# Performance work log

Measured on AMD Instinct MI355X. Metric: run time of the kernel, lower is better.

The kernel has to match this reference:

```python
import jax, jax.numpy as jnp
import numpy as np
import math

T, B, D, H, L, C = 2048, 64, 256, 256, 2, 2
HIGHWAY_BIAS = 0.0
# SRU rescale factor for the highway skip term (rescale=True)
SCALE_X = (1.0 + math.exp(HIGHWAY_BIAS * 2)) ** 0.5


def setup_inputs() -> dict:
    key = jax.random.key(0)
    ks = jax.random.split(key, 8)
    s = 1.0 / np.sqrt(D)
    x = jax.random.normal(ks[0], (T, B, D), dtype=jnp.float32)
    # per-layer SRU weights: W [D, 3H] -> (x_tilde, f, r); bias [2H] -> (b_f, b_r)
    W1 = jax.random.uniform(ks[1], (D, 3 * H), jnp.float32, -s, s)
    b1 = jnp.zeros((2 * H,), jnp.float32)
    W2 = jax.random.uniform(ks[2], (H, 3 * H), jnp.float32, -s, s)
    b2 = jnp.zeros((2 * H,), jnp.float32)
    lin_W = jax.random.uniform(ks[3], (H, C), jnp.float32, -s, s)
    lin_b = jnp.zeros((C,), jnp.float32)
    return {"x": x, "W1": W1, "b1": b1, "W2": W2, "b2": b2,
            "lin_W": lin_W, "lin_b": lin_b}


def _sru_layer(x, W, b):
    # x: [T, B, D]; W: [D, 3H]; b: [2H]. Skip term uses raw x (D == H).
    U = jnp.einsum('tbd,dk->tbk', x, W)           # [T, B, 3H]
    x_tilde, f_raw, r_raw = jnp.split(U, 3, axis=-1)
    b_f, b_r = jnp.split(b, 2)
    f = jax.nn.sigmoid(f_raw + b_f + HIGHWAY_BIAS)  # [T, B, H]
    r = jax.nn.sigmoid(r_raw + b_r)                 # [T, B, H]

    def step(c, inp):
        f_t, xt_t = inp
        c = f_t * c + (1.0 - f_t) * xt_t
        return c, c

    c0 = jnp.zeros(x.shape[1:], x.dtype)            # [B, H]
    _, cs = jax.lax.scan(step, c0, (f, x_tilde))    # cs: [T, B, H]
    h = r * cs + (1.0 - r) * (x * SCALE_X)          # highway skip (rescaled)
    return h


def reference(x, W1, b1, W2, b2, lin_W, lin_b):
    h1 = _sru_layer(x, W1, b1)
    h2 = _sru_layer(h1, W2, b2)
    last = h2[-1]                                   # [B, H] (last timestep)
    # Dropout in eval mode = identity (deterministic reference)
    return last @ lin_W + lin_b                     # [B, C]
```

## Files before the change

kernel.cpp:

```cpp
#include <hip/hip_runtime.h>
#include <hip/hip_bf16.h>
#include <stdint.h>

#define T_LEN 2048
#define B_SZ  64
#define H_SZ  256
#define NH3   768
#define M_SZ  (T_LEN * B_SZ)
#define NC    64
#define TC    32
#define SCALE_X_F 1.41421356237309515f

typedef __attribute__((ext_vector_type(8))) short short8;
typedef __attribute__((ext_vector_type(4))) float f32x4;

__device__ __forceinline__ float sigmoidf_(float z) {
    return 1.0f / (1.0f + __expf(-z));
}
__device__ __forceinline__ unsigned short f2bf(float f) {
    unsigned u = __float_as_uint(f);
    return (unsigned short)((u + 0x7FFFu + ((u >> 16) & 1u)) >> 16);
}
__device__ __forceinline__ float bf2f(unsigned short s) {
    return __uint_as_float(((unsigned)s) << 16);
}

__global__ void k_convert_x(const float* __restrict__ x, unsigned short* __restrict__ xb) {
    int i = blockIdx.x * blockDim.x + threadIdx.x;
    const float4* in = (const float4*)x;
    float4 a = in[i * 2];
    float4 b = in[i * 2 + 1];
    short8 o;
    o[0] = (short)f2bf(a.x); o[1] = (short)f2bf(a.y);
    o[2] = (short)f2bf(a.z); o[3] = (short)f2bf(a.w);
    o[4] = (short)f2bf(b.x); o[5] = (short)f2bf(b.y);
    o[6] = (short)f2bf(b.z); o[7] = (short)f2bf(b.w);
    *(short8*)&xb[(size_t)i * 8] = o;
}

__global__ void k_prep_w(const float* __restrict__ W, unsigned short* __restrict__ Wt) {
    int i = blockIdx.x * 256 + threadIdx.x;
    int n = i >> 8, k = i & 255;
    Wt[i] = f2bf(W[(size_t)k * NH3 + n]);
}

template <int NT, int CS, int TPB>
__global__ void __launch_bounds__(256, 2)
k_gemm(const unsigned short* __restrict__ A,
       const unsigned short* __restrict__ Bt,
       unsigned short* __restrict__ C) {
    __shared__ alignas(16) unsigned short lds[2][16384];

    int orig = blockIdx.x;
    int wgid = (orig & 7) * 64 + (orig >> 3);
    int t0 = wgid * TPB;

    int tid = threadIdx.x;
    int w = tid >> 6, l = tid & 63;
    int r16 = l & 15, kg = l >> 4;
    int wr = w >> 1, wc = w & 1;
    int scol = ((l & 7) ^ (l >> 3)) * 8;
    int srow = (l >> 3);

    auto stage = [&](int t, int kt, int b) {
        int mb = (t / NT) * 128, nb = (t % NT) * 128;
        #pragma unroll
        for (int p = 0; p < 4; ++p) {
            int row = w * 32 + p * 8 + srow;
            const unsigned short* ga = A  + (size_t)(mb + row) * 256 + kt * 64 + scol;
            const unsigned short* gb = Bt + (size_t)(nb + row) * 256 + kt * 64 + scol;
            __builtin_amdgcn_global_load_lds(
                (const __attribute__((address_space(1))) void*)ga,
                (__attribute__((address_space(3))) void*)&lds[b][(w * 4 + p) * 512], 16, 0, 0);
            __builtin_amdgcn_global_load_lds(
                (const __attribute__((address_space(1))) void*)gb,
                (__attribute__((address_space(3))) void*)&lds[b][8192 + (w * 4 + p) * 512], 16, 0, 0);
        }
    };

    stage(t0, 0, 0);

    #pragma unroll 1
    for (int i = 0; i < TPB; ++i) {
        int t = t0 + i;

        f32x4 acc[4][4];
        #pragma unroll
        for (int m = 0; m < 4; ++m)
            #pragma unroll
            for (int n = 0; n < 4; ++n) {
                f32x4 z = {0.f, 0.f, 0.f, 0.f};
                acc[m][n] = z;
            }

        #pragma unroll
        for (int kt = 0; kt < 4; ++kt) {
            if (kt < 3) stage(t, kt + 1, (kt + 1) & 1);
            else        stage(min(t + 1, t0 + TPB - 1), 0, 0);

            asm volatile("s_waitcnt vmcnt(8)" ::: "memory");
            __builtin_amdgcn_s_barrier();
            asm volatile("" ::: "memory");

            const unsigned short* As = &lds[kt & 1][0];
            const unsigned short* Bs = &lds[kt & 1][8192];
            short8 af[4][2], bfv[4][2];
            #pragma unroll
            for (int m = 0; m < 4; ++m) {
                int arow = wr * 64 + m * 16 + r16;
                int sw = (arow & 7) << 3;
                #pragma unroll
                for (int kk = 0; kk < 2; ++kk)
                    af[m][kk] = *(const short8*)&As[arow * 64 + ((kk * 32 + kg * 8) ^ sw)];
            }
            #pragma unroll
            for (int n = 0; n < 4; ++n) {
                int brow = wc * 64 + n * 16 + r16;
                int sw = (brow & 7) << 3;
                #pragma unroll
                for (int kk = 0; kk < 2; ++kk)
                    bfv[n][kk] = *(const short8*)&Bs[brow * 64 + ((kk * 32 + kg * 8) ^ sw)];
            }

            __builtin_amdgcn_s_setprio(1);
            #pragma unroll
            for (int m = 0; m < 4; ++m)
                #pragma unroll
                for (int n = 0; n < 4; ++n)
                    #pragma unroll
                    for (int kk = 0; kk < 2; ++kk)
                        acc[m][n] = __builtin_amdgcn_mfma_f32_16x16x32_bf16(
                            af[m][kk], bfv[n][kk], acc[m][n], 0, 0, 0);
            __builtin_amdgcn_s_setprio(0);

            asm volatile("" ::: "memory");
            __builtin_amdgcn_s_barrier();
            asm volatile("" ::: "memory");
        }

        unsigned short* ep = &lds[1][0];
        int mbase = (t / NT) * 128, nbase = (t % NT) * 128;
        #pragma unroll
        for (int m = 0; m < 4; ++m)
            #pragma unroll
            for (int n = 0; n < 4; ++n) {
                int col = wc * 64 + n * 16 + r16;
                #pragma unroll
                for (int r = 0; r < 4; ++r) {
                    int row = wr * 64 + m * 16 + kg * 4 + r;
                    ep[row * 128 + (col ^ ((row & 7) << 3))] = f2bf(acc[m][n][r]);
                }
            }
        asm volatile("s_waitcnt lgkmcnt(0)" ::: "memory");
        __builtin_amdgcn_s_barrier();
        asm volatile("" ::: "memory");
        #pragma unroll
        for (int s = 0; s < 8; ++s) {
            int slot = s * 256 + tid;
            int row = slot >> 4, seg = slot & 15;
            short8 v = *(const short8*)&ep[row * 128 + ((seg * 8) ^ ((row & 7) << 3))];
            *(short8*)&C[(size_t)(mbase + row) * CS + nbase + seg * 8] = v;
        }
        asm volatile("s_waitcnt lgkmcnt(0)" ::: "memory");
        __builtin_amdgcn_s_barrier();
        asm volatile("" ::: "memory");
    }
}

__global__ void k_passA(const unsigned short* __restrict__ U, const float* __restrict__ bias,
                        float* __restrict__ P, float* __restrict__ S, int stride) {
    int ci = blockIdx.x >> 6;
    int b  = blockIdx.x & 63;
    int h  = threadIdx.x;
    float bfv = bias[h];
    size_t base = ((size_t)(ci * TC) * B_SZ + b) * stride + h;
    float c = 0.f, pr = 1.f;
    #pragma unroll 4
    for (int t = 0; t < TC; ++t) {
        float xt = bf2f(U[base]);
        float fr = bf2f(U[base + 256]);
        float f = sigmoidf_(fr + bfv);
        c = f * c + (1.f - f) * xt;
        pr *= f;
        base += (size_t)B_SZ * stride;
    }
    int o = blockIdx.x * 256 + h;
    P[o] = pr;
    S[o] = c;
}

__global__ void k_passB(const float* __restrict__ P, const float* __restrict__ S,
                        float* __restrict__ cin) {
    int b = blockIdx.x, h = threadIdx.x;
    int idx = b * 256 + h;
    float c = 0.f;
    #pragma unroll 8
    for (int ci = 0; ci < NC; ++ci) {
        cin[ci * 16384 + idx] = c;
        c = P[ci * 16384 + idx] * c + S[ci * 16384 + idx];
    }
    cin[NC * 16384 + idx] = c;
}

__global__ void k_passC(const unsigned short* __restrict__ U, const float* __restrict__ bias,
                        const unsigned short* __restrict__ xb, const float* __restrict__ cin,
                        unsigned short* __restrict__ hout) {
    int ci = blockIdx.x >> 6, b = blockIdx.x & 63, h = threadIdx.x;
    float bfv = bias[h], brv = bias[256 + h];
    float c = cin[blockIdx.x * 256 + h];
    size_t base  = ((size_t)(ci * TC) * B_SZ + b) * NH3 + h;
    size_t xbase = ((size_t)(ci * TC) * B_SZ + b) * H_SZ + h;
    #pragma unroll 4
    for (int t = 0; t < TC; ++t) {
        float xt = bf2f(U[base]);
        float fr = bf2f(U[base + 256]);
        float rr = bf2f(U[base + 512]);
        float f = sigmoidf_(fr + bfv);
        float r = sigmoidf_(rr + brv);
        c = f * c + (1.f - f) * xt;
        float xv = bf2f(xb[xbase]);
        hout[xbase] = f2bf(r * c + (1.f - r) * xv * SCALE_X_F);
        base  += (size_t)B_SZ * NH3;
        xbase += (size_t)B_SZ * H_SZ;
    }
}

__global__ void k_final(const unsigned short* __restrict__ h1, const float* __restrict__ cin,
                        const float* __restrict__ W2, const float* __restrict__ b2,
                        const float* __restrict__ lw, const float* __restrict__ lb,
                        float* __restrict__ out) {
    int b = blockIdx.x, h = threadIdx.x;
    __shared__ float hrow[256];
    size_t hb = ((size_t)(T_LEN - 1) * B_SZ + b) * H_SZ;
    hrow[h] = bf2f(h1[hb + h]);
    __syncthreads();
    float rr = 0.f;
    #pragma unroll 8
    for (int k = 0; k < 256; ++k)
        rr += hrow[k] * W2[(size_t)k * NH3 + 512 + h];
    float r = sigmoidf_(rr + b2[256 + h]);
    float c = cin[NC * 16384 + b * 256 + h];
    float hv = r * c + (1.f - r) * hrow[h] * SCALE_X_F;
    float p0 = hv * lw[h * 2];
    float p1 = hv * lw[h * 2 + 1];
    #pragma unroll
    for (int off = 32; off; off >>= 1) {
        p0 += __shfl_down(p0, off);
        p1 += __shfl_down(p1, off);
    }
    __shared__ float s0[4], s1[4];
    int wid = h >> 6, lane = h & 63;
    if (lane == 0) { s0[wid] = p0; s1[wid] = p1; }
    __syncthreads();
    if (h == 0) {
        out[b * 2]     = s0[0] + s0[1] + s0[2] + s0[3] + lb[0];
        out[b * 2 + 1] = s1[0] + s1[1] + s1[2] + s1[3] + lb[1];
    }
}

extern "C" void kernel_launch(void* const* d_in, const int* in_sizes, int n_in,
                              void* d_out, int out_size, void* d_ws, size_t ws_size,
                              hipStream_t stream) {
    const float* x   = (const float*)d_in[0];
    const float* W1  = (const float*)d_in[1];
    const float* b1  = (const float*)d_in[2];
    const float* W2  = (const float*)d_in[3];
    const float* b2  = (const float*)d_in[4];
    const float* lw  = (const float*)d_in[5];
    const float* lb  = (const float*)d_in[6];
    float* out = (float*)d_out;

    char* ws = (char*)d_ws;
    unsigned short* U   = (unsigned short*)ws;
    unsigned short* xb  = (unsigned short*)(ws + 201326592);
    unsigned short* h1  = (unsigned short*)(ws + 268435456);
    unsigned short* Wt1 = (unsigned short*)(ws + 335544320);
    unsigned short* Wt2 = (unsigned short*)(ws + 335937536);
    float* Pbuf = (float*)(ws + 336330752);
    float* Sbuf = (float*)(ws + 340525056);
    float* cin  = (float*)(ws + 344719360);

    k_convert_x<<<16384, 256, 0, stream>>>(x, xb);
    k_prep_w<<<768, 256, 0, stream>>>(W1, Wt1);
    k_prep_w<<<512, 256, 0, stream>>>(W2, Wt2);

    k_gemm<6, NH3, 12><<<512, 256, 0, stream>>>(xb, Wt1, U);
    k_passA<<<4096, 256, 0, stream>>>(U, b1, Pbuf, Sbuf, NH3);
    k_passB<<<64, 256, 0, stream>>>(Pbuf, Sbuf, cin);
    k_passC<<<4096, 256, 0, stream>>>(U, b1, xb, cin, h1);

    k_gemm<4, 512, 8><<<512, 256, 0, stream>>>(h1, Wt2, U);
    k_passA<<<4096, 256, 0, stream>>>(U, b2, Pbuf, Sbuf, 512);
    k_passB<<<64, 256, 0, stream>>>(Pbuf, Sbuf, cin);
    k_final<<<64, 256, 0, stream>>>(h1, cin, W2, b2, lw, lb, out);
}
```

Before: 347.4 us.

## Restructure GEMM to triple-buffered K=32 stages with persistent XCD-aware tile scheduling

The bf16 GEMM kernel moves from double-buffered 64-wide K slices to a three-buffer ring of 32-wide K slices, which cuts LDS per workgroup and lets three workgroups share a CU. Tiles are now handed out round-robin inside each XCD from a persistent grid of 768 blocks instead of a fixed contiguous run per block. The epilogue writes through a half-size staging buffer in two passes. The intent is deeper prefetch, higher occupancy and better load balance, at the cost of more barriers per tile and more complex waitcnt bookkeeping.

```diff
diff --git a/kernel.cpp b/kernel.cpp
--- a/kernel.cpp
+++ b/kernel.cpp
@@ -44,45 +44,50 @@
     Wt[i] = f2bf(W[(size_t)k * NH3 + n]);
 }
 
-template <int NT, int CS, int TPB>
-__global__ void __launch_bounds__(256, 2)
+template <int NT, int CS, int TPX>
+__global__ void __launch_bounds__(256, 3)
 k_gemm(const unsigned short* __restrict__ A,
        const unsigned short* __restrict__ Bt,
        unsigned short* __restrict__ C) {
-    __shared__ alignas(16) unsigned short lds[2][16384];
+    __shared__ alignas(16) unsigned short lds[3][8192];
 
     int orig = blockIdx.x;
-    int wgid = (orig & 7) * 64 + (orig >> 3);
-    int t0 = wgid * TPB;
+    int xcd = orig & 7, b_in = orig >> 3;
+    int ntiles = (TPX - b_in + 95) / 96;
 
     int tid = threadIdx.x;
     int w = tid >> 6, l = tid & 63;
     int r16 = l & 15, kg = l >> 4;
     int wr = w >> 1, wc = w & 1;
-    int scol = ((l & 7) ^ (l >> 3)) * 8;
-    int srow = (l >> 3);
-
-    auto stage = [&](int t, int kt, int b) {
-        int mb = (t / NT) * 128, nb = (t % NT) * 128;
-        #pragma unroll
-        for (int p = 0; p < 4; ++p) {
-            int row = w * 32 + p * 8 + srow;
-            const unsigned short* ga = A  + (size_t)(mb + row) * 256 + kt * 64 + scol;
-            const unsigned short* gb = Bt + (size_t)(nb + row) * 256 + kt * 64 + scol;
+    int srow = l >> 2;
+    int schunk = ((l & 3) ^ (srow & 3)) * 8;
+
+    auto stage = [&](int mb, int nb, int kt, unsigned short* buf) {
+        #pragma unroll
+        for (int p = 0; p < 2; ++p) {
+            int row = w * 32 + p * 16 + srow;
+            const unsigned short* ga = A  + (size_t)(mb + row) * 256 + kt * 32 + schunk;
+            const unsigned short* gb = Bt + (size_t)(nb + row) * 256 + kt * 32 + schunk;
             __builtin_amdgcn_global_load_lds(
                 (const __attribute__((address_space(1))) void*)ga,
-                (__attribute__((address_space(3))) void*)&lds[b][(w * 4 + p) * 512], 16, 0, 0);
+                (__attribute__((address_space(3))) void*)(buf + (w * 2 + p) * 512), 16, 0, 0);
             __builtin_amdgcn_global_load_lds(
                 (const __attribute__((address_space(1))) void*)gb,
-                (__attribute__((address_space(3))) void*)&lds[b][8192 + (w * 4 + p) * 512], 16, 0, 0);
+                (__attribute__((address_space(3))) void*)(buf + 4096 + (w * 2 + p) * 512), 16, 0, 0);
         }
     };
 
-    stage(t0, 0, 0);
-
-    #pragma unroll 1
-    for (int i = 0; i < TPB; ++i) {
-        int t = t0 + i;
+    unsigned short *p0 = &lds[0][0], *p1 = &lds[1][0], *p2 = &lds[2][0];
+
+    int tau = b_in;
+    int mbase = (xcd * 128 + tau / NT) * 128, nbase = (tau % NT) * 128;
+
+    stage(mbase, nbase, 0, p0);
+    stage(mbase, nbase, 1, p1);
+
+    for (int j = 0; j < ntiles; ++j) {
+        int tau_n = (j + 1 < ntiles) ? tau + 96 : tau;
+        int mb_n = (xcd * 128 + tau_n / NT) * 128, nb_n = (tau_n % NT) * 128;
 
         f32x4 acc[4][4];
         #pragma unroll
@@ -94,32 +99,27 @@
             }
 
         #pragma unroll
-        for (int kt = 0; kt < 4; ++kt) {
-            if (kt < 3) stage(t, kt + 1, (kt + 1) & 1);
-            else        stage(min(t + 1, t0 + TPB - 1), 0, 0);
-
-            asm volatile("s_waitcnt vmcnt(8)" ::: "memory");
+        for (int k = 0; k < 8; ++k) {
+            if (k < 2) {
+                if (j == 0) { asm volatile("s_waitcnt vmcnt(4)" ::: "memory"); }
+                else        { asm volatile("s_waitcnt vmcnt(12)" ::: "memory"); }
+            } else        { asm volatile("s_waitcnt vmcnt(4)" ::: "memory"); }
             __builtin_amdgcn_s_barrier();
             asm volatile("" ::: "memory");
 
-            const unsigned short* As = &lds[kt & 1][0];
-            const unsigned short* Bs = &lds[kt & 1][8192];
-            short8 af[4][2], bfv[4][2];
+            if (k < 6) stage(mbase, nbase, k + 2, p2);
+            else       stage(mb_n, nb_n, k - 6, p2);
+
+            short8 af[4], bfv[4];
             #pragma unroll
             for (int m = 0; m < 4; ++m) {
                 int arow = wr * 64 + m * 16 + r16;
-                int sw = (arow & 7) << 3;
-                #pragma unroll
-                for (int kk = 0; kk < 2; ++kk)
-                    af[m][kk] = *(const short8*)&As[arow * 64 + ((kk * 32 + kg * 8) ^ sw)];
+                af[m] = *(const short8*)&p0[arow * 32 + ((kg ^ (arow & 3)) * 8)];
             }
             #pragma unroll
             for (int n = 0; n < 4; ++n) {
                 int brow = wc * 64 + n * 16 + r16;
-                int sw = (brow & 7) << 3;
-                #pragma unroll
-                for (int kk = 0; kk < 2; ++kk)
-                    bfv[n][kk] = *(const short8*)&Bs[brow * 64 + ((kk * 32 + kg * 8) ^ sw)];
+                bfv[n] = *(const short8*)&p0[4096 + brow * 32 + ((kg ^ (brow & 3)) * 8)];
             }
 
             __builtin_amdgcn_s_setprio(1);
@@ -127,43 +127,45 @@
             for (int m = 0; m < 4; ++m)
                 #pragma unroll
                 for (int n = 0; n < 4; ++n)
+                    acc[m][n] = __builtin_amdgcn_mfma_f32_16x16x32_bf16(
+                        af[m], bfv[n], acc[m][n], 0, 0, 0);
+            __builtin_amdgcn_s_setprio(0);
+
+            unsigned short* t = p0; p0 = p1; p1 = p2; p2 = t;
+        }
+
+        unsigned short* ep = p2;
+        #pragma unroll
+        for (int pass = 0; pass < 2; ++pass) {
+            asm volatile("" ::: "memory");
+            __builtin_amdgcn_s_barrier();
+            asm volatile("" ::: "memory");
+            if (wr == pass) {
+                #pragma unroll
+                for (int m = 0; m < 4; ++m)
                     #pragma unroll
-                    for (int kk = 0; kk < 2; ++kk)
-                        acc[m][n] = __builtin_amdgcn_mfma_f32_16x16x32_bf16(
-                            af[m][kk], bfv[n][kk], acc[m][n], 0, 0, 0);
-            __builtin_amdgcn_s_setprio(0);
-
-            asm volatile("" ::: "memory");
+                    for (int n = 0; n < 4; ++n) {
+                        int col = wc * 64 + n * 16 + r16;
+                        #pragma unroll
+                        for (int r = 0; r < 4; ++r) {
+                            int row = m * 16 + kg * 4 + r;
+                            ep[row * 128 + (col ^ ((row & 7) << 3))] = f2bf(acc[m][n][r]);
+                        }
+                    }
+            }
+            asm volatile("s_waitcnt lgkmcnt(0)" ::: "memory");
             __builtin_amdgcn_s_barrier();
             asm volatile("" ::: "memory");
+            #pragma unroll
+            for (int s = 0; s < 4; ++s) {
+                int slot = s * 256 + tid;
+                int row = slot >> 4, seg = slot & 15;
+                short8 v = *(const short8*)&ep[row * 128 + ((seg * 8) ^ ((row & 7) << 3))];
+                *(short8*)&C[(size_t)(mbase + pass * 64 + row) * CS + nbase + seg * 8] = v;
+            }
         }
 
-        unsigned short* ep = &lds[1][0];
-        int mbase = (t / NT) * 128, nbase = (t % NT) * 128;
-        #pragma unroll
-        for (int m = 0; m < 4; ++m)
-            #pragma unroll
-            for (int n = 0; n < 4; ++n) {
-                int col = wc * 64 + n * 16 + r16;
-                #pragma unroll
-                for (int r = 0; r < 4; ++r) {
-                    int row = wr * 64 + m * 16 + kg * 4 + r;
-                    ep[row * 128 + (col ^ ((row & 7) << 3))] = f2bf(acc[m][n][r]);
-                }
-            }
-        asm volatile("s_waitcnt lgkmcnt(0)" ::: "memory");
-        __builtin_amdgcn_s_barrier();
-        asm volatile("" ::: "memory");
-        #pragma unroll
-        for (int s = 0; s < 8; ++s) {
-            int slot = s * 256 + tid;
-            int row = slot >> 4, seg = slot & 15;
-            short8 v = *(const short8*)&ep[row * 128 + ((seg * 8) ^ ((row & 7) << 3))];
-            *(short8*)&C[(size_t)(mbase + row) * CS + nbase + seg * 8] = v;
-        }
-        asm volatile("s_waitcnt lgkmcnt(0)" ::: "memory");
-        __builtin_amdgcn_s_barrier();
-        asm volatile("" ::: "memory");
+        tau = tau_n; mbase = mb_n; nbase = nb_n;
     }
 }
 
@@ -284,12 +286,12 @@
     k_prep_w<<<768, 256, 0, stream>>>(W1, Wt1);
     k_prep_w<<<512, 256, 0, stream>>>(W2, Wt2);
 
-    k_gemm<6, NH3, 12><<<512, 256, 0, stream>>>(xb, Wt1, U);
+    k_gemm<6, NH3, 768><<<768, 256, 0, stream>>>(xb, Wt1, U);
     k_passA<<<4096, 256, 0, stream>>>(U, b1, Pbuf, Sbuf, NH3);
     k_passB<<<64, 256, 0, stream>>>(Pbuf, Sbuf, cin);
     k_passC<<<4096, 256, 0, stream>>>(U, b1, xb, cin, h1);
 
-    k_gemm<4, 512, 8><<<512, 256, 0, stream>>>(h1, Wt2, U);
+    k_gemm<4, 512, 512><<<768, 256, 0, stream>>>(h1, Wt2, U);
     k_passA<<<4096, 256, 0, stream>>>(U, b2, Pbuf, Sbuf, 512);
     k_passB<<<64, 256, 0, stream>>>(Pbuf, Sbuf, cin);
     k_final<<<64, 256, 0, stream>>>(h1, cin, W2, b2, lw, lb, out);
```

After: 551.7 us. 58.8% more time.
